# Kernel optimization log

Hardware: AMD Instinct MI355X
Metric: run time of the kernel (lower is better)

## Reference

```python
import jax, jax.numpy as jnp
import numpy as np


def _lstm(x, W_ih, W_hh, b_ih, b_hh):
    """PyTorch-semantics LSTM over [B, T, F] -> [B, T, H]. Gate order: i, f, g, o."""
    H = W_hh.shape[1]
    # Precompute input projection for all timesteps: [B, T, 4H]
    xg = jnp.einsum('btf,gf->btg', x, W_ih) + b_ih + b_hh
    xg = jnp.transpose(xg, (1, 0, 2))  # time-major [T, B, 4H]
    B = x.shape[0]
    h0 = jnp.zeros((B, H), dtype=x.dtype)
    c0 = jnp.zeros((B, H), dtype=x.dtype)

    def step(carry, xt):
        h, c = carry
        gates = xt + h @ W_hh.T  # [B, 4H]
        i, f, g, o = jnp.split(gates, 4, axis=-1)
        i = jax.nn.sigmoid(i)
        f = jax.nn.sigmoid(f)
        g = jnp.tanh(g)
        o = jax.nn.sigmoid(o)
        c = f * c + i * g
        h = o * jnp.tanh(c)
        return (h, c), h

    _, hs = jax.lax.scan(step, (h0, c0), xg)
    return jnp.transpose(hs, (1, 0, 2))  # [B, T, H]


def setup_inputs() -> dict:
    key = jax.random.key(0)
    ks = jax.random.split(key, 16)
    B, T, F = 4096, 256, 32
    H1, H2, D1 = 64, 32, 16
    s1 = 1.0 / np.sqrt(H1)
    s2 = 1.0 / np.sqrt(H2)
    inp = {
        'x': jax.random.normal(ks[0], (B, T, F), dtype=jnp.float32),
        'W_ih1': jax.random.uniform(ks[1], (4 * H1, F), jnp.float32, -s1, s1),
        'W_hh1': jax.random.uniform(ks[2], (4 * H1, H1), jnp.float32, -s1, s1),
        'b_ih1': jax.random.uniform(ks[3], (4 * H1,), jnp.float32, -s1, s1),
        'b_hh1': jax.random.uniform(ks[4], (4 * H1,), jnp.float32, -s1, s1),
        'W_ih2': jax.random.uniform(ks[5], (4 * H2, H1), jnp.float32, -s2, s2),
        'W_hh2': jax.random.uniform(ks[6], (4 * H2, H2), jnp.float32, -s2, s2),
        'b_ih2': jax.random.uniform(ks[7], (4 * H2,), jnp.float32, -s2, s2),
        'b_hh2': jax.random.uniform(ks[8], (4 * H2,), jnp.float32, -s2, s2),
        'W_fc1': jax.random.uniform(ks[9], (D1, H2), jnp.float32, -s2, s2),
        'b_fc1': jax.random.uniform(ks[10], (D1,), jnp.float32, -s2, s2),
        'W_fc2': jax.random.uniform(ks[11], (1, D1), jnp.float32, -0.25, 0.25),
        'b_fc2': jax.random.uniform(ks[12], (1,), jnp.float32, -0.25, 0.25),
    }
    return inp


def reference(x, W_ih1, W_hh1, b_ih1, b_hh1, W_ih2, W_hh2, b_ih2, b_hh2,
              W_fc1, b_fc1, W_fc2, b_fc2):
    # Dropout is identity in eval/inference mode.
    h = _lstm(x, W_ih1, W_hh1, b_ih1, b_hh1)        # [B, T, 64]
    h = _lstm(h, W_ih2, W_hh2, b_ih2, b_hh2)        # [B, T, 32]
    h = h[:, -1, :]                                  # [B, 32]
    h = jax.nn.relu(h @ W_fc1.T + b_fc1)             # [B, 16]
    out = h @ W_fc2.T + b_fc2                        # [B, 1]
    return out.squeeze(-1)                           # [B]
```

## Files before the change

kernel.cpp:

```cpp
#include <hip/hip_runtime.h>

#define T_   256
#define F_   32
#define NBB  16
#define TPB  512
#define IMW  136

typedef __attribute__((ext_vector_type(8))) short bf16x8;
typedef __attribute__((ext_vector_type(4))) float f32x4;
typedef __attribute__((ext_vector_type(4))) unsigned short ush4;

#define K1f  (-1.44269504f)
#define K2f  (-2.88539008f)

__device__ __forceinline__ unsigned short bf16_rne(float x){
    unsigned u = __float_as_uint(x);
    u += 0x7FFF + ((u >> 16) & 1);
    return (unsigned short)(u >> 16);
}
__device__ __forceinline__ void bf16_split(float x, unsigned short& h, unsigned short& l){
    h = bf16_rne(x);
    float xr = __uint_as_float(((unsigned)h) << 16);
    l = bf16_rne(x - xr);
}
__device__ __forceinline__ void make_frags_s(const float* __restrict__ p8, float s,
                                             bf16x8& fh, bf16x8& fl){
    #pragma unroll
    for (int e = 0; e < 8; ++e){
        unsigned short h, l; bf16_split(s * p8[e], h, l);
        fh[e] = (short)h; fl[e] = (short)l;
    }
}
__device__ __forceinline__ float sigm_pre(float p){
    return __builtin_amdgcn_rcpf(1.f + __builtin_amdgcn_exp2f(p));
}
__device__ __forceinline__ float tanh_pre(float p){
    return fmaf(2.f, __builtin_amdgcn_rcpf(1.f + __builtin_amdgcn_exp2f(p)), -1.f);
}
__device__ __forceinline__ float unit_combine(float gi, float gf, float gg, float go, float& c){
    const float i_ = sigm_pre(gi);
    const float f_ = sigm_pre(gf);
    const float g_ = tanh_pre(gg);
    const float o_ = sigm_pre(go);
    c = fmaf(f_, c, i_ * g_);
    return o_ * tanh_pre(K2f * c);
}

#define MFMA(A,B,C) __builtin_amdgcn_mfma_f32_16x16x32_bf16((A),(B),(C),0,0,0)

__device__ __forceinline__ void step_barrier(){
    asm volatile("s_waitcnt lgkmcnt(0)" ::: "memory");
    __builtin_amdgcn_s_barrier();
}

__global__ __launch_bounds__(TPB, 2) void lstm_mfma(
    const float* __restrict__ x,
    const float* __restrict__ W_ih1,
    const float* __restrict__ W_hh1,
    const float* __restrict__ b_ih1,
    const float* __restrict__ b_hh1,
    const float* __restrict__ W_ih2,
    const float* __restrict__ W_hh2,
    const float* __restrict__ b_ih2,
    const float* __restrict__ b_hh2,
    const float* __restrict__ W_fc1,
    const float* __restrict__ b_fc1,
    const float* __restrict__ W_fc2,
    const float* __restrict__ b_fc2,
    float* __restrict__ out)
{
    const int tid  = threadIdx.x;
    const int lane = tid & 63;
    const int wid  = tid >> 6;
    const int bb   = lane & 15;
    const int kg   = (lane >> 4) & 3;
    const int b0   = blockIdx.x * NBB;

    __shared__ __align__(16) unsigned short i12[2][NBB][IMW];
    __shared__ float hfin[NBB][32];
    __shared__ float hd[NBB][16];

    bf16x8 wh[4][3], wl[4][3];
    f32x4  bfr[4];
    if (wid < 4){
        #pragma unroll
        for (int g = 0; g < 4; ++g){
            const float s = (g == 2) ? K2f : K1f;
            const int r = 64*g + 16*wid + bb;
            make_frags_s(&W_ih1[r*32 +      8*kg], s, wh[g][0], wl[g][0]);
            make_frags_s(&W_hh1[r*64 +      8*kg], s, wh[g][1], wl[g][1]);
            make_frags_s(&W_hh1[r*64 + 32 + 8*kg], s, wh[g][2], wl[g][2]);
            #pragma unroll
            for (int q = 0; q < 4; ++q){
                const int row = 64*g + 16*wid + 4*kg + q;
                bfr[g][q] = s * (b_ih1[row] + b_hh1[row]);
            }
        }
    } else if (wid < 6){
        const int j = wid - 4;
        #pragma unroll
        for (int g = 0; g < 4; ++g){
            const float s = (g == 2) ? K2f : K1f;
            const int r = 32*g + 16*j + bb;
            make_frags_s(&W_ih2[r*64 +      8*kg], s, wh[g][0], wl[g][0]);
            make_frags_s(&W_ih2[r*64 + 32 + 8*kg], s, wh[g][1], wl[g][1]);
            make_frags_s(&W_hh2[r*32 +      8*kg], s, wh[g][2], wl[g][2]);
            #pragma unroll
            for (int q = 0; q < 4; ++q){
                const int row = 32*g + 16*j + 4*kg + q;
                bfr[g][q] = s * (b_ih2[row] + b_hh2[row]);
            }
        }
    }

    float cc[4] = {0.f, 0.f, 0.f, 0.f};

    const int xt  = tid & 127;
    const int xcb = xt >> 3;
    const int xf  = (xt & 7) * 4;
    const size_t xbase = (size_t)(b0 + xcb) * (T_*F_) + xf;
    float4 xc = make_float4(0.f, 0.f, 0.f, 0.f);

    for (int i = tid; i < 2*NBB*IMW; i += TPB) (&i12[0][0][0])[i] = 0;
    __syncthreads();
    if (wid >= 6){
        float4 x0 = *(const float4*)&x[xbase];
        ush4 HH;
        HH[0] = bf16_rne(x0.x); HH[1] = bf16_rne(x0.y);
        HH[2] = bf16_rne(x0.z); HH[3] = bf16_rne(x0.w);
        *(ush4*)&i12[0][xcb][xf] = HH;
        xc = *(const float4*)&x[xbase + F_];
    }
    __syncthreads();

    for (int t = 0; t <= T_; ++t){
        const int cur = t & 1, nxt = cur ^ 1;

        if (wid < 4){
            if (t < T_){
                const unsigned short* ph = &i12[cur][0][0] + bb*IMW + 8*kg;
                bf16x8 vh[3];
                #pragma unroll
                for (int kb = 0; kb < 3; ++kb)
                    vh[kb] = *(const bf16x8*)(ph + 32*kb);
                f32x4 a0 = bfr[0], a1 = bfr[1], a2 = bfr[2], a3 = bfr[3];
                #pragma unroll
                for (int kb = 0; kb < 3; ++kb){
                    a0 = MFMA(wh[0][kb], vh[kb], a0);
                    a1 = MFMA(wh[1][kb], vh[kb], a1);
                    a2 = MFMA(wh[2][kb], vh[kb], a2);
                    a3 = MFMA(wh[3][kb], vh[kb], a3);
                }
                #pragma unroll
                for (int kb = 0; kb < 3; ++kb){
                    a0 = MFMA(wl[0][kb], vh[kb], a0);
                    a1 = MFMA(wl[1][kb], vh[kb], a1);
                    a2 = MFMA(wl[2][kb], vh[kb], a2);
                    a3 = MFMA(wl[3][kb], vh[kb], a3);
                }
                ush4 HH;
                #pragma unroll
                for (int q = 0; q < 4; ++q){
                    const float h = unit_combine(a0[q], a1[q], a2[q], a3[q], cc[q]);
                    HH[q] = bf16_rne(h);
                }
                *(ush4*)&i12[nxt][bb][32 + 16*wid + 4*kg] = HH;
            }
        } else if (wid < 6){
            if (t >= 1){
                const unsigned short* ph = &i12[cur][0][0] + bb*IMW + 32 + 8*kg;
                bf16x8 vh[3];
                #pragma unroll
                for (int kb = 0; kb < 3; ++kb)
                    vh[kb] = *(const bf16x8*)(ph + 32*kb);
                f32x4 a0 = bfr[0], a1 = bfr[1], a2 = bfr[2], a3 = bfr[3];
                #pragma unroll
                for (int kb = 0; kb < 3; ++kb){
                    a0 = MFMA(wh[0][kb], vh[kb], a0);
                    a1 = MFMA(wh[1][kb], vh[kb], a1);
                    a2 = MFMA(wh[2][kb], vh[kb], a2);
                    a3 = MFMA(wh[3][kb], vh[kb], a3);
                }
                #pragma unroll
                for (int kb = 0; kb < 3; ++kb){
                    a0 = MFMA(wl[0][kb], vh[kb], a0);
                    a1 = MFMA(wl[1][kb], vh[kb], a1);
                    a2 = MFMA(wl[2][kb], vh[kb], a2);
                    a3 = MFMA(wl[3][kb], vh[kb], a3);
                }
                const int j = wid - 4;
                ush4 HH;
                float hv[4];
                #pragma unroll
                for (int q = 0; q < 4; ++q){
                    hv[q] = unit_combine(a0[q], a1[q], a2[q], a3[q], cc[q]);
                    HH[q] = bf16_rne(hv[q]);
                }
                *(ush4*)&i12[nxt][bb][96 + 16*j + 4*kg] = HH;
                if (t - 1 == T_ - 1){
                    const int u = 16*j + 4*kg;
                    hfin[bb][u]   = hv[0]; hfin[bb][u+1] = hv[1];
                    hfin[bb][u+2] = hv[2]; hfin[bb][u+3] = hv[3];
                }
            }
        } else {
            if (t + 1 < T_){
                ush4 HH;
                HH[0] = bf16_rne(xc.x); HH[1] = bf16_rne(xc.y);
                HH[2] = bf16_rne(xc.z); HH[3] = bf16_rne(xc.w);
                *(ush4*)&i12[nxt][xcb][xf] = HH;
                const int tn = (t + 2 < T_) ? t + 2 : T_ - 1;
                xc = *(const float4*)&x[xbase + (size_t)tn * F_];
            }
        }
        step_barrier();
    }

    __syncthreads();
    if (tid < NBB * 16){
        const int b = tid >> 4, j2 = tid & 15;
        float a = b_fc1[j2];
        #pragma unroll
        for (int kk = 0; kk < 32; ++kk) a = fmaf(W_fc1[j2*32 + kk], hfin[b][kk], a);
        hd[b][j2] = fmaxf(a, 0.f);
    }
    __syncthreads();
    if (tid < NBB){
        float a = b_fc2[0];
        #pragma unroll
        for (int kk = 0; kk < 16; ++kk) a = fmaf(W_fc2[kk], hd[tid][kk], a);
        out[b0 + tid] = a;
    }
}

extern "C" void kernel_launch(void* const* d_in, const int* in_sizes, int n_in,
                              void* d_out, int out_size, void* d_ws, size_t ws_size,
                              hipStream_t stream) {
    const float* x     = (const float*)d_in[0];
    const float* W_ih1 = (const float*)d_in[1];
    const float* W_hh1 = (const float*)d_in[2];
    const float* b_ih1 = (const float*)d_in[3];
    const float* b_hh1 = (const float*)d_in[4];
    const float* W_ih2 = (const float*)d_in[5];
    const float* W_hh2 = (const float*)d_in[6];
    const float* b_ih2 = (const float*)d_in[7];
    const float* b_hh2 = (const float*)d_in[8];
    const float* W_fc1 = (const float*)d_in[9];
    const float* b_fc1 = (const float*)d_in[10];
    const float* W_fc2 = (const float*)d_in[11];
    const float* b_fc2 = (const float*)d_in[12];
    float* out = (float*)d_out;

    const int B = in_sizes[0] / (T_ * F_);
    dim3 grid(B / NBB), block(TPB);
    hipLaunchKernelGGL(lstm_mfma, grid, block, 0, stream,
                       x, W_ih1, W_hh1, b_ih1, b_hh1,
                       W_ih2, W_hh2, b_ih2, b_hh2,
                       W_fc1, b_fc1, W_fc2, b_fc2, out);
}
```

Before: 228.7 us.

## Halve batch rows per block and fold x-loader waves into layer-2 waves

Each block now handles 8 batch rows instead of 16 and runs 6 waves instead of 8. The two dedicated x-loader waves are removed and their work moves into the layer-2 waves, with each thread loading float2 instead of float4. MFMA tiles still compute 16 columns, but lanes 8-15 read duplicated rows and their results are discarded. The aim is more blocks (512 instead of 256) and better spread across CUs for the latency-bound recurrence, at the cost of half-wasted MFMA work and extra load work on the layer-2 critical path.

```diff
diff --git a/kernel.cpp b/kernel.cpp
--- a/kernel.cpp
+++ b/kernel.cpp
@@ -2,8 +2,8 @@
 
 #define T_   256
 #define F_   32
-#define NBB  16
-#define TPB  512
+#define NBB  8
+#define TPB  384
 #define IMW  136
 
 typedef __attribute__((ext_vector_type(8))) short bf16x8;
@@ -53,7 +53,8 @@
     __builtin_amdgcn_s_barrier();
 }
 
-__global__ __launch_bounds__(TPB, 2) void lstm_mfma(
+__global__ __launch_bounds__(TPB) __attribute__((amdgpu_waves_per_eu(3, 3)))
+void lstm_mfma(
     const float* __restrict__ x,
     const float* __restrict__ W_ih1,
     const float* __restrict__ W_hh1,
@@ -73,6 +74,7 @@
     const int lane = tid & 63;
     const int wid  = tid >> 6;
     const int bb   = lane & 15;
+    const int bbm  = bb & 7;
     const int kg   = (lane >> 4) & 3;
     const int b0   = blockIdx.x * NBB;
 
@@ -96,7 +98,7 @@
                 bfr[g][q] = s * (b_ih1[row] + b_hh1[row]);
             }
         }
-    } else if (wid < 6){
+    } else {
         const int j = wid - 4;
         #pragma unroll
         for (int g = 0; g < 4; ++g){
@@ -116,20 +118,18 @@
     float cc[4] = {0.f, 0.f, 0.f, 0.f};
 
     const int xt  = tid & 127;
-    const int xcb = xt >> 3;
-    const int xf  = (xt & 7) * 4;
+    const int xcb = xt >> 4;
+    const int xf  = (xt & 15) * 2;
     const size_t xbase = (size_t)(b0 + xcb) * (T_*F_) + xf;
-    float4 xc = make_float4(0.f, 0.f, 0.f, 0.f);
+    float2 xc = make_float2(0.f, 0.f);
 
     for (int i = tid; i < 2*NBB*IMW; i += TPB) (&i12[0][0][0])[i] = 0;
     __syncthreads();
-    if (wid >= 6){
-        float4 x0 = *(const float4*)&x[xbase];
-        ush4 HH;
-        HH[0] = bf16_rne(x0.x); HH[1] = bf16_rne(x0.y);
-        HH[2] = bf16_rne(x0.z); HH[3] = bf16_rne(x0.w);
-        *(ush4*)&i12[0][xcb][xf] = HH;
-        xc = *(const float4*)&x[xbase + F_];
+    if (wid >= 4){
+        float2 x0 = *(const float2*)&x[xbase];
+        *(unsigned*)&i12[0][xcb][xf] =
+            (unsigned)bf16_rne(x0.x) | ((unsigned)bf16_rne(x0.y) << 16);
+        xc = *(const float2*)&x[xbase + F_];
     }
     __syncthreads();
 
@@ -138,7 +138,7 @@
 
         if (wid < 4){
             if (t < T_){
-                const unsigned short* ph = &i12[cur][0][0] + bb*IMW + 8*kg;
+                const unsigned short* ph = &i12[cur][0][0] + bbm*IMW + 8*kg;
                 bf16x8 vh[3];
                 #pragma unroll
                 for (int kb = 0; kb < 3; ++kb)
@@ -164,11 +164,18 @@
                     const float h = unit_combine(a0[q], a1[q], a2[q], a3[q], cc[q]);
                     HH[q] = bf16_rne(h);
                 }
-                *(ush4*)&i12[nxt][bb][32 + 16*wid + 4*kg] = HH;
-            }
-        } else if (wid < 6){
+                if (bb < NBB)
+                    *(ush4*)&i12[nxt][bb][32 + 16*wid + 4*kg] = HH;
+            }
+        } else {
+            if (t + 1 < T_){
+                *(unsigned*)&i12[nxt][xcb][xf] =
+                    (unsigned)bf16_rne(xc.x) | ((unsigned)bf16_rne(xc.y) << 16);
+                const int tn = (t + 2 < T_) ? t + 2 : T_ - 1;
+                xc = *(const float2*)&x[xbase + (size_t)tn * F_];
+            }
             if (t >= 1){
-                const unsigned short* ph = &i12[cur][0][0] + bb*IMW + 32 + 8*kg;
+                const unsigned short* ph = &i12[cur][0][0] + bbm*IMW + 32 + 8*kg;
                 bf16x8 vh[3];
                 #pragma unroll
                 for (int kb = 0; kb < 3; ++kb)
@@ -196,21 +203,14 @@
                     hv[q] = unit_combine(a0[q], a1[q], a2[q], a3[q], cc[q]);
                     HH[q] = bf16_rne(hv[q]);
                 }
-                *(ush4*)&i12[nxt][bb][96 + 16*j + 4*kg] = HH;
-                if (t - 1 == T_ - 1){
-                    const int u = 16*j + 4*kg;
-                    hfin[bb][u]   = hv[0]; hfin[bb][u+1] = hv[1];
-                    hfin[bb][u+2] = hv[2]; hfin[bb][u+3] = hv[3];
-                }
-            }
-        } else {
-            if (t + 1 < T_){
-                ush4 HH;
-                HH[0] = bf16_rne(xc.x); HH[1] = bf16_rne(xc.y);
-                HH[2] = bf16_rne(xc.z); HH[3] = bf16_rne(xc.w);
-                *(ush4*)&i12[nxt][xcb][xf] = HH;
-                const int tn = (t + 2 < T_) ? t + 2 : T_ - 1;
-                xc = *(const float4*)&x[xbase + (size_t)tn * F_];
+                if (bb < NBB){
+                    *(ush4*)&i12[nxt][bb][96 + 16*j + 4*kg] = HH;
+                    if (t - 1 == T_ - 1){
+                        const int u = 16*j + 4*kg;
+                        hfin[bb][u]   = hv[0]; hfin[bb][u+1] = hv[1];
+                        hfin[bb][u+2] = hv[2]; hfin[bb][u+3] = hv[3];
+                    }
+                }
             }
         }
         step_barrier();
```

Measured after the change: 453.7 us. 98.4% more time.
